# Kernel tuning notes

Hardware: AMD Instinct MI355X
Metric: run time of the kernel (lower is better)

## Reference

```python
import jax, jax.numpy as jnp
import numpy as np

E = 1024      # embedding_size
K = 64        # key_size
D = 64        # head_size
S = 1024      # context_size
V = 32000     # vocab_size
H = 16        # layer_size (heads per layer)
L = 8         # num_layers
B = 2


def _pe():
    pos = jnp.arange(S, dtype=jnp.float32)[:, None]
    i = jnp.arange(E, dtype=jnp.float32)[None, :]
    ang = pos / jnp.power(10000.0, 2.0 * i / E)
    return jnp.where((jnp.arange(E) % 2 == 0)[None, :], jnp.sin(ang), jnp.cos(ang))


def setup_inputs() -> dict:
    key = jax.random.key(0)
    ks = iter(jax.random.split(key, 32))
    s = 0.02
    n = lambda shape: jax.random.normal(next(ks), shape, dtype=jnp.float32) * s
    inp = {
        "tokens": jax.random.randint(next(ks), (B, S), 0, V),
        "emb": n((V, E)),
        "pe": _pe(),
        "k1w": n((L, H, K, E)), "k1b": n((L, H, K)),
        "k2w": n((L, H, K, K)), "k2b": n((L, H, K)),
        "q1w": n((L, H, K, E)), "q1b": n((L, H, K)),
        "q2w": n((L, H, K, K)), "q2b": n((L, H, K)),
        "vw": n((L, H, D, E)), "vb": n((L, H, D)),
        "lnw": jnp.ones((L, E), jnp.float32), "lnb": jnp.zeros((L, E), jnp.float32),
        "p1w": n((L, E, E)), "p1b": n((L, E)),
        "p2w": n((L, E, E)), "p2b": n((L, E)),
        "predw": n((V, E)), "predb": n((V,)),
    }
    return inp


def reference(tokens, emb, pe, k1w, k1b, k2w, k2b, q1w, q1b, q2w, q2b,
              vw, vb, lnw, lnb, p1w, p1b, p2w, p2b, predw, predb):
    relu = jax.nn.relu
    x = emb[tokens] + pe[:tokens.shape[1]]                       # [B,S,E]
    seq = tokens.shape[1]
    # Faithful to original: tril (past+diag) gets the -1e10 penalty.
    mask = jnp.tril(jnp.ones((seq, seq), x.dtype)) * -1e10
    for l in range(L):
        # two-layer ReLU MLPs for K and Q, batched over heads
        k = relu(jnp.einsum('bse,hke->bhsk', x, k1w[l]) + k1b[l][None, :, None, :])
        k = relu(jnp.einsum('bhsk,hjk->bhsj', k, k2w[l]) + k2b[l][None, :, None, :])
        q = relu(jnp.einsum('bse,hke->bhsk', x, q1w[l]) + q1b[l][None, :, None, :])
        q = relu(jnp.einsum('bhsk,hjk->bhsj', q, q2w[l]) + q2b[l][None, :, None, :])
        v = jnp.einsum('bse,hde->bhsd', x, vw[l]) + vb[l][None, :, None, :]
        scores = jnp.einsum('bhsk,bhtk->bhst', q, k) / (K ** 0.5) + mask
        w = jax.nn.softmax(scores, axis=-1)
        o = jnp.einsum('bhst,bhtd->bhsd', w, v)                  # [B,H,S,D]
        o = o.transpose(0, 2, 1, 3).reshape(x.shape[0], seq, H * D)
        y = x + o
        mu = y.mean(-1, keepdims=True)
        var = ((y - mu) ** 2).mean(-1, keepdims=True)
        yn = (y - mu) / jnp.sqrt(var + 1e-5) * lnw[l] + lnb[l]
        h1 = relu(yn @ p1w[l].T + p1b[l])
        x = relu(h1 @ p2w[l].T + p2b[l])
    logits = x @ predw.T + predb                                 # [B,S,V]
    return logits
```

## Files before the change

### kernel.cpp

```cpp
#include <hip/hip_runtime.h>


typedef __attribute__((ext_vector_type(8))) short bf16x8;
typedef __attribute__((ext_vector_type(4))) float f32x4;

#define L_ 8
#define S_ 1024
#define E_ 1024
#define B_ 2
#define H_ 16
#define V_ 32000
#define M_ 2048

__device__ __forceinline__ unsigned short f2b(float f) {
  union { float f; unsigned int u; } v; v.f = f;
  unsigned int r = v.u + 0x7FFFu + ((v.u >> 16) & 1u);
  return (unsigned short)(r >> 16);
}

#define GLDS16(gptr, lptr)                                                            \
  __builtin_amdgcn_global_load_lds(                                                   \
      (const __attribute__((address_space(1))) unsigned int*)(gptr),                  \
      (__attribute__((address_space(3))) unsigned int*)(lptr), 16, 0, 0)

__global__ void cvt_all_kernel(
    const float* __restrict__ k1w, const float* __restrict__ q1w,
    const float* __restrict__ vw,  const float* __restrict__ k2w,
    const float* __restrict__ q2w, const float* __restrict__ p1w,
    const float* __restrict__ p2w, const float* __restrict__ predw,
    unsigned short* __restrict__ wcat, unsigned short* __restrict__ wk2,
    unsigned short* __restrict__ wq2,  unsigned short* __restrict__ wp1,
    unsigned short* __restrict__ wp2,  unsigned short* __restrict__ wpred) {
  size_t u = (size_t)blockIdx.x * 256 + threadIdx.x;
  const float* src; unsigned short* dst;
  if (u < 6291456) {
    int seg = (int)(u / 2097152);
    size_t e0 = (u - (size_t)seg * 2097152) * 4;
    const float* s = (seg == 0) ? k1w : (seg == 1) ? q1w : vw;
    src = s + e0;
    int l = (int)(e0 >> 20), off = (int)(e0 & 1048575);
    dst = wcat + (size_t)l * 3145728 + (size_t)seg * 1048576 + off;
  } else if (u < 6422528) { size_t e = (u - 6291456) * 4;  src = k2w + e;   dst = wk2 + e; }
  else if (u < 6553600)   { size_t e = (u - 6422528) * 4;  src = q2w + e;   dst = wq2 + e; }
  else if (u < 8650752)   { size_t e = (u - 6553600) * 4;  src = p1w + e;   dst = wp1 + e; }
  else if (u < 10747904)  { size_t e = (u - 8650752) * 4;  src = p2w + e;   dst = wp2 + e; }
  else                    { size_t e = (u - 10747904) * 4; src = predw + e; dst = wpred + e; }
  float4 v = *(const float4*)src;
  dst[0] = f2b(v.x); dst[1] = f2b(v.y); dst[2] = f2b(v.z); dst[3] = f2b(v.w);
}

__global__ void biascat_kernel(const float* __restrict__ k1b, const float* __restrict__ q1b,
                               const float* __restrict__ vb, float* __restrict__ bcat) {
  int i = blockIdx.x * 256 + threadIdx.x;
  int l = i / 3072, j = i - l * 3072;
  float v;
  if (j < 1024)      v = k1b[l * 1024 + j];
  else if (j < 2048) v = q1b[l * 1024 + j - 1024];
  else               v = vb [l * 1024 + j - 2048];
  bcat[i] = v;
}

__global__ void embed_kernel(const int* __restrict__ tokens, const float* __restrict__ emb,
                             const float* __restrict__ pe, float* __restrict__ x32,
                             unsigned short* __restrict__ xb) {
  int row = blockIdx.x;
  int s = row & (S_ - 1);
  int e0 = threadIdx.x * 4;
  int tok = tokens[row];
  float4 ev = *(const float4*)(emb + (size_t)tok * E_ + e0);
  float4 pv = *(const float4*)(pe + (size_t)s * E_ + e0);
  float4 v; v.x = ev.x + pv.x; v.y = ev.y + pv.y; v.z = ev.z + pv.z; v.w = ev.w + pv.w;
  *(float4*)(x32 + (size_t)row * E_ + e0) = v;
  ushort4 o; o.x = f2b(v.x); o.y = f2b(v.y); o.z = f2b(v.z); o.w = f2b(v.w);
  *(ushort4*)(xb + (size_t)row * E_ + e0) = o;
}

template <int BM, int BN, int RELU, int OBF, int OF32, int VT>
__global__ __launch_bounds__(256) void gemm97(
    const unsigned short* __restrict__ A, const unsigned short* __restrict__ W,
    const float* __restrict__ bias, unsigned short* __restrict__ Cb,
    float* __restrict__ Cf, unsigned short* __restrict__ vTp,
    int K, int N, int reluN) {
  constexpr int AR = BM / 64;
  constexpr int BR = BN / 64;
  constexpr int FM = BM / 32;
  constexpr int FN = BN / 32;
  __shared__ __align__(16) unsigned short sA[BM * 32];
  __shared__ __align__(16) unsigned short sB[BN * 32];
  const int tid = threadIdx.x;
  const int lane = tid & 63, wave = tid >> 6;
  const int l16 = lane & 15, lhi = lane >> 4;

  const int gx = gridDim.x, nwg = gx * gridDim.y;
  int o = blockIdx.y * gx + blockIdx.x;
  int wg = ((nwg & 7) == 0) ? ((o & 7) * (nwg >> 3) + (o >> 3)) : o;
  const int row0 = (wg % gx) * BM, col0 = (wg / gx) * BN;

  const int wm = (wave >> 1) * (BM / 2), wn = (wave & 1) * (BN / 2);

  const int srow = wave * 16 + (lane >> 2);
  const int scol = ((lane & 3) ^ ((lane >> 3) & 3)) * 8;
  const int cx = (lhi ^ ((l16 >> 1) & 3)) * 8;

  f32x4 acc[FM][FN] = {};

  for (int k0 = 0; k0 < K; k0 += 32) {
#pragma unroll
    for (int r = 0; r < AR; r++)
      GLDS16(A + (size_t)(row0 + r * 64 + srow) * K + k0 + scol,
             sA + r * 2048 + wave * 512);
#pragma unroll
    for (int r = 0; r < BR; r++)
      GLDS16(W + (size_t)(col0 + r * 64 + srow) * K + k0 + scol,
             sB + r * 2048 + wave * 512);
    __syncthreads();

    bf16x8 af[FM], bf[FN];
#pragma unroll
    for (int i = 0; i < FM; i++)
      af[i] = *(const bf16x8*)(sA + (wm + i * 16 + l16) * 32 + cx);
#pragma unroll
    for (int j = 0; j < FN; j++)
      bf[j] = *(const bf16x8*)(sB + (wn + j * 16 + l16) * 32 + cx);
#pragma unroll
    for (int i = 0; i < FM; i++)
#pragma unroll
      for (int j = 0; j < FN; j++)
        acc[i][j] = __builtin_amdgcn_mfma_f32_16x16x32_bf16(bf[j], af[i], acc[i][j], 0, 0, 0);
    __syncthreads();
  }

#pragma unroll
  for (int j = 0; j < FN; j++) {
    const int colb = col0 + wn + j * 16 + lhi * 4;
    const float4 bv = *(const float4*)(bias + colb);
    const bool dorelu = (RELU == 1) || (RELU == 2 && colb < reluN);
#pragma unroll
    for (int i = 0; i < FM; i++) {
      const int row = row0 + wm + i * 16 + l16;
      float v0 = acc[i][j][0] + bv.x, v1 = acc[i][j][1] + bv.y;
      float v2 = acc[i][j][2] + bv.z, v3 = acc[i][j][3] + bv.w;
      if (dorelu) {
        v0 = fmaxf(v0, 0.f); v1 = fmaxf(v1, 0.f);
        v2 = fmaxf(v2, 0.f); v3 = fmaxf(v3, 0.f);
      }
      if (OBF) {
        ushort4 ob; ob.x = f2b(v0); ob.y = f2b(v1); ob.z = f2b(v2); ob.w = f2b(v3);
        *(ushort4*)(Cb + (size_t)row * N + colb) = ob;
      }
      if (OF32) {
        float4 of; of.x = v0; of.y = v1; of.z = v2; of.w = v3;
        *(float4*)(Cf + (size_t)row * N + colb) = of;
      }
      if (VT) {
        if (colb - lhi * 4 >= 2048) {
          const int hd0 = colb - 2048;
          const int bq = row >> 10, s = row & 1023;
          unsigned short* vr = vTp + ((size_t)(bq << 10) + hd0) * 1024 + s;
          vr[0] = f2b(v0); vr[1024] = f2b(v1); vr[2048] = f2b(v2); vr[3072] = f2b(v3);
        }
      }
    }
  }
}

__global__ __launch_bounds__(512, 1) void gemm256_8p(
    const unsigned short* __restrict__ A, const unsigned short* __restrict__ W,
    const float* __restrict__ bias, float* __restrict__ Cf) {
  constexpr int NT = 16;
  __shared__ __align__(16) unsigned short sA[2][2][8192];
  __shared__ __align__(16) unsigned short sB[2][2][8192];
  const int tid = threadIdx.x;
  const int lane = tid & 63, wave = tid >> 6;
  const int l16 = lane & 15, lhi = lane >> 4;
  const int wr = wave >> 2, wc = wave & 3;

  const int o = blockIdx.x;
  const int wg = (o & 7) * 125 + (o >> 3);
  const int row0 = (wg & 7) * 256;
  const int col0 = (wg >> 3) * 256;

  const int srow = tid >> 2;
  const int sk   = ((tid & 3) ^ ((tid >> 2) & 3)) * 8;
  const int rsw  = (l16 & 3);

  f32x4 acc[2][4][4] = {};

  auto stageA = [&](int kt, int s) {
    const int buf = kt & 1;
    const int kg = kt * 64 + s * 32 + sk;
#pragma unroll
    for (int i = 0; i < 2; i++)
      GLDS16(A + (size_t)(row0 + i * 128 + srow) * 1024 + kg,
             &sA[buf][s][i * 4096 + wave * 512]);
  };
  auto stageB = [&](int kt, int s) {
    const int buf = kt & 1;
    const int kg = kt * 64 + s * 32 + sk;
#pragma unroll
    for (int i = 0; i < 2; i++)
      GLDS16(W + (size_t)(col0 + i * 128 + srow) * 1024 + kg,
             &sB[buf][s][i * 4096 + wave * 512]);
  };

  stageA(0, 0); stageB(0, 0); stageA(0, 1); stageB(0, 1);

  bf16x8 af[4], bf[4];
  for (int kt = 0; kt < NT; kt++) {
    const int buf = kt & 1;
    const bool more = (kt + 1 < NT);

    asm volatile("s_waitcnt vmcnt(4)" ::: "memory");
    __builtin_amdgcn_s_barrier();
    __builtin_amdgcn_sched_barrier(0);
#pragma unroll
    for (int j = 0; j < 4; j++)
      bf[j] = *(const bf16x8*)(&sB[buf][0][(wc * 64 + j * 16 + l16) * 32 + ((lhi ^ rsw) << 3)]);
#pragma unroll
    for (int i = 0; i < 4; i++)
      af[i] = *(const bf16x8*)(&sA[buf][0][(wr * 128 + i * 16 + l16) * 32 + ((lhi ^ rsw) << 3)]);
    if (more) stageA(kt + 1, 0);
    asm volatile("s_waitcnt lgkmcnt(0)" ::: "memory");
    __builtin_amdgcn_sched_barrier(0);
    __builtin_amdgcn_s_setprio(1);
#pragma unroll
    for (int i = 0; i < 4; i++)
#pragma unroll
      for (int j = 0; j < 4; j++)
        acc[0][i][j] = __builtin_amdgcn_mfma_f32_16x16x32_bf16(bf[j], af[i], acc[0][i][j], 0, 0, 0);
    __builtin_amdgcn_s_setprio(0);
    __builtin_amdgcn_s_barrier();

#pragma unroll
    for (int i = 0; i < 4; i++)
      af[i] = *(const bf16x8*)(&sA[buf][0][(wr * 128 + 64 + i * 16 + l16) * 32 + ((lhi ^ rsw) << 3)]);
    if (more) stageB(kt + 1, 0);
    asm volatile("s_waitcnt lgkmcnt(0)" ::: "memory");
    __builtin_amdgcn_sched_barrier(0);
    __builtin_amdgcn_s_setprio(1);
#pragma unroll
    for (int i = 0; i < 4; i++)
#pragma unroll
      for (int j = 0; j < 4; j++)
        acc[1][i][j] = __builtin_amdgcn_mfma_f32_16x16x32_bf16(bf[j], af[i], acc[1][i][j], 0, 0, 0);
    __builtin_amdgcn_s_setprio(0);
    __builtin_amdgcn_s_barrier();

    if (kt == NT - 1) { asm volatile("s_waitcnt vmcnt(0)" ::: "memory"); }
    else              { asm volatile("s_waitcnt vmcnt(4)" ::: "memory"); }
    __builtin_amdgcn_s_barrier();
    __builtin_amdgcn_sched_barrier(0);
#pragma unroll
    for (int j = 0; j < 4; j++)
      bf[j] = *(const bf16x8*)(&sB[buf][1][(wc * 64 + j * 16 + l16) * 32 + ((lhi ^ rsw) << 3)]);
#pragma unroll
    for (int i = 0; i < 4; i++)
      af[i] = *(const bf16x8*)(&sA[buf][1][(wr * 128 + i * 16 + l16) * 32 + ((lhi ^ rsw) << 3)]);
    if (more) stageA(kt + 1, 1);
    asm volatile("s_waitcnt lgkmcnt(0)" ::: "memory");
    __builtin_amdgcn_sched_barrier(0);
    __builtin_amdgcn_s_setprio(1);
#pragma unroll
    for (int i = 0; i < 4; i++)
#pragma unroll
      for (int j = 0; j < 4; j++)
        acc[0][i][j] = __builtin_amdgcn_mfma_f32_16x16x32_bf16(bf[j], af[i], acc[0][i][j], 0, 0, 0);
    __builtin_amdgcn_s_setprio(0);
    __builtin_amdgcn_s_barrier();

#pragma unroll
    for (int i = 0; i < 4; i++)
      af[i] = *(const bf16x8*)(&sA[buf][1][(wr * 128 + 64 + i * 16 + l16) * 32 + ((lhi ^ rsw) << 3)]);
    if (more) stageB(kt + 1, 1);
    asm volatile("s_waitcnt lgkmcnt(0)" ::: "memory");
    __builtin_amdgcn_sched_barrier(0);
    __builtin_amdgcn_s_setprio(1);
#pragma unroll
    for (int i = 0; i < 4; i++)
#pragma unroll
      for (int j = 0; j < 4; j++)
        acc[1][i][j] = __builtin_amdgcn_mfma_f32_16x16x32_bf16(bf[j], af[i], acc[1][i][j], 0, 0, 0);
    __builtin_amdgcn_s_setprio(0);
    __builtin_amdgcn_s_barrier();
  }

#pragma unroll
  for (int rh = 0; rh < 2; rh++) {
#pragma unroll
    for (int j = 0; j < 4; j++) {
      const int colb = col0 + wc * 64 + j * 16 + lhi * 4;
      const float4 bv = *(const float4*)(bias + colb);
#pragma unroll
      for (int i = 0; i < 4; i++) {
        const int row = row0 + wr * 128 + rh * 64 + i * 16 + l16;
        float4 of;
        of.x = acc[rh][i][j][0] + bv.x; of.y = acc[rh][i][j][1] + bv.y;
        of.z = acc[rh][i][j][2] + bv.z; of.w = acc[rh][i][j][3] + bv.w;
        *(float4*)(Cf + (size_t)row * V_ + colb) = of;
      }
    }
  }
}

__global__ __launch_bounds__(256) void k2q2_kernel(
    const unsigned short* __restrict__ kqv, const unsigned short* __restrict__ wk2,
    const unsigned short* __restrict__ wq2, const float* __restrict__ k2b,
    const float* __restrict__ q2b, unsigned short* __restrict__ kbuf,
    unsigned short* __restrict__ qbuf) {
  const int m0 = blockIdx.x * 64;
  const int h = blockIdx.y;
  const int which = blockIdx.z;
  const unsigned short* Ap = kqv + (which ? 1024 : 0) + h * 64;
  const unsigned short* Wp = (which ? wq2 : wk2) + h * 4096;
  const float* bias = (which ? q2b : k2b) + h * 64;
  unsigned short* out = (which ? qbuf : kbuf) + h * 64;
  const int lane = threadIdx.x & 63, wave = threadIdx.x >> 6;
  const int l16 = lane & 15, lhi = lane >> 4;
  const int mw = m0 + wave * 16;

  f32x4 acc[4] = {};
#pragma unroll
  for (int ks = 0; ks < 2; ks++) {
    bf16x8 a = *(const bf16x8*)(Ap + (size_t)(mw + l16) * 3072 + ks * 32 + (lhi << 3));
#pragma unroll
    for (int j = 0; j < 4; j++) {
      bf16x8 b = *(const bf16x8*)(Wp + (j * 16 + l16) * 64 + ks * 32 + (lhi << 3));
      acc[j] = __builtin_amdgcn_mfma_f32_16x16x32_bf16(a, b, acc[j], 0, 0, 0);
    }
  }
#pragma unroll
  for (int j = 0; j < 4; j++) {
    float bv = bias[j * 16 + l16];
#pragma unroll
    for (int r = 0; r < 4; r++) {
      int row = mw + (lhi << 2) + r;
      float v = fmaxf(acc[j][r] + bv, 0.f);
      out[(size_t)row * 1024 + j * 16 + l16] = f2b(v);
    }
  }
}

__global__ __launch_bounds__(128) void attn_kernel(
    const unsigned short* __restrict__ qbuf,
    const unsigned short* __restrict__ kbuf,
    const unsigned short* __restrict__ vT,
    float* __restrict__ o32) {
  constexpr int LD = 72;
  __shared__ __align__(16) unsigned short sP[2 * 16 * LD];
  const int bid = blockIdx.x;
  const int bh = bid & 31, qt = bid >> 5;
  const int b = bh >> 4, h = bh & 15;
  const int tid = threadIdx.x, lane = tid & 63, w = tid >> 6;
  const int l16 = lane & 15, lhi = lane >> 4;
  const int base = b * S_;
  const int qrow = qt * 32 + w * 16 + l16;

  bf16x8 aq[2];
#pragma unroll
  for (int ks = 0; ks < 2; ks++)
    aq[ks] = *(const bf16x8*)(qbuf + (size_t)(base + qrow) * 1024 + h * 64 + ks * 32 + (lhi << 3));

  f32x4 oacc[4] = {};
  float psum[4] = {0.f, 0.f, 0.f, 0.f};
  const int srow = qt * 32 + w * 16 + (lhi << 2);
  const int t0s = (qt == 31) ? 0 : ((qt >> 1) << 6);

  unsigned short* sPw = sP + w * 16 * LD;

  bf16x8 kA[8], vA[8], kB[8], vB[8];

  auto loadKV = [&](int t0, bf16x8* kd, bf16x8* vd) {
#pragma unroll
    for (int nt = 0; nt < 4; nt++) {
#pragma unroll
      for (int ks = 0; ks < 2; ks++) {
        kd[nt * 2 + ks] = *(const bf16x8*)(kbuf + (size_t)(base + t0 + nt * 16 + l16) * 1024 +
                                           h * 64 + ks * 32 + (lhi << 3));
        vd[nt * 2 + ks] = *(const bf16x8*)(vT + (size_t)(bh * 64 + nt * 16 + l16) * 1024 +
                                           t0 + ks * 32 + (lhi << 3));
      }
    }
  };

  auto compute = [&](int t0, const bf16x8* kc, const bf16x8* vc) {
    f32x4 sacc[4] = {};
#pragma unroll
    for (int ks = 0; ks < 2; ks++)
#pragma unroll
      for (int nt = 0; nt < 4; nt++)
        sacc[nt] = __builtin_amdgcn_mfma_f32_16x16x32_bf16(aq[ks], kc[nt * 2 + ks], sacc[nt], 0, 0, 0);
#pragma unroll
    for (int nt = 0; nt < 4; nt++) {
      int tcol = t0 + nt * 16 + l16;
#pragma unroll
      for (int r = 0; r < 4; r++) {
        const int row = srow + r;
        float e;
        if (row == S_ - 1)      e = 1.f;
        else if (tcol <= row)   e = 0.f;
        else                    e = __expf(fminf(sacc[nt][r] * 0.125f, 60.f));
        psum[r] += e;
        sPw[((lhi << 2) + r) * LD + nt * 16 + l16] = f2b(e);
      }
    }
#pragma unroll
    for (int ks = 0; ks < 2; ks++) {
      bf16x8 ap = *(const bf16x8*)(sPw + l16 * LD + ks * 32 + (lhi << 3));
#pragma unroll
      for (int nt = 0; nt < 4; nt++)
        oacc[nt] = __builtin_amdgcn_mfma_f32_16x16x32_bf16(ap, vc[nt * 2 + ks], oacc[nt], 0, 0, 0);
    }
  };

  loadKV(t0s, kA, vA);
  int t0 = t0s;
  while (true) {
    if (t0 + 64 < S_) loadKV(t0 + 64, kB, vB);
    compute(t0, kA, vA);
    t0 += 64; if (t0 >= S_) break;
    if (t0 + 64 < S_) loadKV(t0 + 64, kA, vA);
    compute(t0, kB, vB);
    t0 += 64; if (t0 >= S_) break;
  }

  float lrun[4];
#pragma unroll
  for (int r = 0; r < 4; r++) {
    float rs = psum[r];
#pragma unroll
    for (int off = 1; off < 16; off <<= 1) rs += __shfl_xor(rs, off, 16);
    lrun[r] = rs;
  }
#pragma unroll
  for (int nt = 0; nt < 4; nt++) {
#pragma unroll
    for (int r = 0; r < 4; r++) {
      int row = srow + r;
      o32[(size_t)(base + row) * 1024 + h * 64 + nt * 16 + l16] = oacc[nt][r] / lrun[r];
    }
  }
}

__global__ __launch_bounds__(256) void ln_kernel(
    const float* __restrict__ x32, const float* __restrict__ o32,
    const float* __restrict__ lnw, const float* __restrict__ lnb,
    unsigned short* __restrict__ yn) {
  __shared__ float red[8];
  const int row = blockIdx.x, tid = threadIdx.x;
  const int lane = tid & 63, wave = tid >> 6;
  const int e0 = tid * 4;
  float4 xv = *(const float4*)(x32 + (size_t)row * E_ + e0);
  float4 ov = *(const float4*)(o32 + (size_t)row * E_ + e0);
  float y0 = xv.x + ov.x, y1 = xv.y + ov.y, y2 = xv.z + ov.z, y3 = xv.w + ov.w;
  float s = y0 + y1 + y2 + y3;
  float sq = y0 * y0 + y1 * y1 + y2 * y2 + y3 * y3;
#pragma unroll
  for (int off = 32; off > 0; off >>= 1) {
    s += __shfl_xor(s, off, 64);
    sq += __shfl_xor(sq, off, 64);
  }
  if (lane == 0) { red[wave * 2] = s; red[wave * 2 + 1] = sq; }
  __syncthreads();
  float ts = red[0] + red[2] + red[4] + red[6];
  float tsq = red[1] + red[3] + red[5] + red[7];
  float mu = ts * (1.f / E_);
  float var = tsq * (1.f / E_) - mu * mu;
  float rstd = rsqrtf(var + 1e-5f);
  float4 gv = *(const float4*)(lnw + e0);
  float4 bv = *(const float4*)(lnb + e0);
  ushort4 o;
  o.x = f2b((y0 - mu) * rstd * gv.x + bv.x);
  o.y = f2b((y1 - mu) * rstd * gv.y + bv.y);
  o.z = f2b((y2 - mu) * rstd * gv.z + bv.z);
  o.w = f2b((y3 - mu) * rstd * gv.w + bv.w);
  *(ushort4*)(yn + (size_t)row * E_ + e0) = o;
}

extern "C" void kernel_launch(void* const* d_in, const int* in_sizes, int n_in,
                              void* d_out, int out_size, void* d_ws, size_t ws_size,
                              hipStream_t stream) {
  const int* tokens  = (const int*)d_in[0];
  const float* emb   = (const float*)d_in[1];
  const float* pe    = (const float*)d_in[2];
  const float* k1w   = (const float*)d_in[3];
  const float* k1b   = (const float*)d_in[4];
  const float* k2w   = (const float*)d_in[5];
  const float* k2b   = (const float*)d_in[6];
  const float* q1w   = (const float*)d_in[7];
  const float* q1b   = (const float*)d_in[8];
  const float* q2w   = (const float*)d_in[9];
  const float* q2b   = (const float*)d_in[10];
  const float* vw    = (const float*)d_in[11];
  const float* vb    = (const float*)d_in[12];
  const float* lnw   = (const float*)d_in[13];
  const float* lnb   = (const float*)d_in[14];
  const float* p1w   = (const float*)d_in[15];
  const float* p1b   = (const float*)d_in[16];
  const float* p2w   = (const float*)d_in[17];
  const float* p2b   = (const float*)d_in[18];
  const float* predw = (const float*)d_in[19];
  const float* predb = (const float*)d_in[20];
  float* out = (float*)d_out;

  char* p = (char*)d_ws;
  auto alloc = [&](size_t bytes) -> char* {
    char* r = p; p += (bytes + 255) & ~(size_t)255; return r;
  };
  unsigned short* wcat  = (unsigned short*)alloc((size_t)L_ * 3072 * 1024 * 2);
  unsigned short* wk2   = (unsigned short*)alloc((size_t)L_ * H_ * 64 * 64 * 2);
  unsigned short* wq2   = (unsigned short*)alloc((size_t)L_ * H_ * 64 * 64 * 2);
  unsigned short* wp1   = (unsigned short*)alloc((size_t)L_ * 1024 * 1024 * 2);
  unsigned short* wp2   = (unsigned short*)alloc((size_t)L_ * 1024 * 1024 * 2);
  unsigned short* wpred = (unsigned short*)alloc((size_t)V_ * 1024 * 2);
  float*          bcat  = (float*)alloc((size_t)L_ * 3072 * 4);
  float*          x32   = (float*)alloc((size_t)M_ * 1024 * 4);
  unsigned short* xb    = (unsigned short*)alloc((size_t)M_ * 1024 * 2);
  unsigned short* kqv   = (unsigned short*)alloc((size_t)M_ * 3072 * 2);
  unsigned short* kbuf  = (unsigned short*)alloc((size_t)M_ * 1024 * 2);
  unsigned short* qbuf  = (unsigned short*)alloc((size_t)M_ * 1024 * 2);
  unsigned short* vTb   = (unsigned short*)alloc((size_t)32 * 64 * 1024 * 2);
  float*          o32   = (float*)alloc((size_t)M_ * 1024 * 4);
  unsigned short* yn    = (unsigned short*)alloc((size_t)M_ * 1024 * 2);
  unsigned short* h1    = (unsigned short*)alloc((size_t)M_ * 1024 * 2);
  if ((size_t)(p - (char*)d_ws) > ws_size) return;

  cvt_all_kernel<<<73984, 256, 0, stream>>>(k1w, q1w, vw, k2w, q2w, p1w, p2w, predw,
                                            wcat, wk2, wq2, wp1, wp2, wpred);
  biascat_kernel<<<96, 256, 0, stream>>>(k1b, q1b, vb, bcat);

  embed_kernel<<<M_, 256, 0, stream>>>(tokens, emb, pe, x32, xb);

  for (int l = 0; l < L_; l++) {
    const unsigned short* wcat_l = wcat + (size_t)l * 3072 * 1024;
    const float* bcat_l = bcat + (size_t)l * 3072;
    const unsigned short* wk2_l = wk2 + (size_t)l * H_ * 64 * 64;
    const unsigned short* wq2_l = wq2 + (size_t)l * H_ * 64 * 64;
    const unsigned short* wp1_l = wp1 + (size_t)l * 1024 * 1024;
    const unsigned short* wp2_l = wp2 + (size_t)l * 1024 * 1024;

    gemm97<128, 128, 2, 1, 0, 1><<<dim3(16, 24), 256, 0, stream>>>(
        xb, wcat_l, bcat_l, kqv, nullptr, vTb, 1024, 3072, 2048);
    k2q2_kernel<<<dim3(32, 16, 2), 256, 0, stream>>>(
        kqv, wk2_l, wq2_l, k2b + l * 1024, q2b + l * 1024, kbuf, qbuf);
    attn_kernel<<<1024, 128, 0, stream>>>(qbuf, kbuf, vTb, o32);
    ln_kernel<<<M_, 256, 0, stream>>>(x32, o32, lnw + l * 1024, lnb + l * 1024, yn);
    gemm97<64, 128, 1, 1, 0, 0><<<dim3(32, 8), 256, 0, stream>>>(
        yn, wp1_l, p1b + l * 1024, h1, nullptr, nullptr, 1024, 1024, 0);
    gemm97<64, 128, 1, 1, 1, 0><<<dim3(32, 8), 256, 0, stream>>>(
        h1, wp2_l, p2b + l * 1024, xb, x32, nullptr, 1024, 1024, 0);
  }

  gemm256_8p<<<1000, 512, 0, stream>>>(xb, wpred, predb, out);
}
```

Baseline: 1.457 ms.

## Fuse second K/Q MLP layer into the KQV projection GEMM epilogue

```diff
diff --git a/kernel.cpp b/kernel.cpp
--- a/kernel.cpp
+++ b/kernel.cpp
@@ -75,11 +75,14 @@
   *(ushort4*)(xb + (size_t)row * E_ + e0) = o;
 }
 
-template <int BM, int BN, int RELU, int OBF, int OF32, int VT>
+template <int BM, int BN, int RELU, int OBF, int OF32, int VT, int K2Q2>
 __global__ __launch_bounds__(256) void gemm97(
     const unsigned short* __restrict__ A, const unsigned short* __restrict__ W,
     const float* __restrict__ bias, unsigned short* __restrict__ Cb,
     float* __restrict__ Cf, unsigned short* __restrict__ vTp,
+    const unsigned short* __restrict__ wk2p, const unsigned short* __restrict__ wq2p,
+    const float* __restrict__ k2bp, const float* __restrict__ q2bp,
+    unsigned short* __restrict__ kbufp, unsigned short* __restrict__ qbufp,
     int K, int N, int reluN) {
   constexpr int AR = BM / 64;
   constexpr int BR = BN / 64;
@@ -87,6 +90,7 @@
   constexpr int FN = BN / 32;
   __shared__ __align__(16) unsigned short sA[BM * 32];
   __shared__ __align__(16) unsigned short sB[BN * 32];
+  __shared__ __align__(16) unsigned short sC[K2Q2 ? 128 * 136 : 1];
   const int tid = threadIdx.x;
   const int lane = tid & 63, wave = tid >> 6;
   const int l16 = lane & 15, lhi = lane >> 4;
@@ -130,34 +134,90 @@
     __syncthreads();
   }
 
-#pragma unroll
-  for (int j = 0; j < FN; j++) {
-    const int colb = col0 + wn + j * 16 + lhi * 4;
-    const float4 bv = *(const float4*)(bias + colb);
-    const bool dorelu = (RELU == 1) || (RELU == 2 && colb < reluN);
-#pragma unroll
-    for (int i = 0; i < FM; i++) {
-      const int row = row0 + wm + i * 16 + l16;
-      float v0 = acc[i][j][0] + bv.x, v1 = acc[i][j][1] + bv.y;
-      float v2 = acc[i][j][2] + bv.z, v3 = acc[i][j][3] + bv.w;
-      if (dorelu) {
-        v0 = fmaxf(v0, 0.f); v1 = fmaxf(v1, 0.f);
-        v2 = fmaxf(v2, 0.f); v3 = fmaxf(v3, 0.f);
+  if (K2Q2 && col0 < 2048) {
+#pragma unroll
+    for (int j = 0; j < FN; j++) {
+      const int colb = wn + j * 16 + lhi * 4;
+      const float4 bv = *(const float4*)(bias + col0 + colb);
+#pragma unroll
+      for (int i = 0; i < FM; i++) {
+        const int lrow = wm + i * 16 + l16;
+        ushort4 ob;
+        ob.x = f2b(fmaxf(acc[i][j][0] + bv.x, 0.f));
+        ob.y = f2b(fmaxf(acc[i][j][1] + bv.y, 0.f));
+        ob.z = f2b(fmaxf(acc[i][j][2] + bv.z, 0.f));
+        ob.w = f2b(fmaxf(acc[i][j][3] + bv.w, 0.f));
+        *(ushort4*)(sC + lrow * 136 + colb) = ob;
       }
-      if (OBF) {
-        ushort4 ob; ob.x = f2b(v0); ob.y = f2b(v1); ob.z = f2b(v2); ob.w = f2b(v3);
-        *(ushort4*)(Cb + (size_t)row * N + colb) = ob;
+    }
+    __syncthreads();
+    const int which = (col0 >= 1024) ? 1 : 0;
+    const int h = ((col0 & 1023) >> 6) + (wave & 1);
+    const unsigned short* W2 = (which ? wq2p : wk2p) + h * 4096;
+    const float* b2 = (which ? q2bp : k2bp) + h * 64;
+    unsigned short* outp = (which ? qbufp : kbufp) + h * 64;
+    const int r0 = (wave >> 1) * 64;
+    f32x4 acc2[4][4] = {};
+#pragma unroll
+    for (int ks = 0; ks < 2; ks++) {
+      bf16x8 bfr[4], af2[4];
+#pragma unroll
+      for (int j = 0; j < 4; j++)
+        bfr[j] = *(const bf16x8*)(W2 + (j * 16 + l16) * 64 + ks * 32 + (lhi << 3));
+#pragma unroll
+      for (int i = 0; i < 4; i++)
+        af2[i] = *(const bf16x8*)(sC + (r0 + i * 16 + l16) * 136 + (wave & 1) * 64 +
+                                  ks * 32 + (lhi << 3));
+#pragma unroll
+      for (int i = 0; i < 4; i++)
+#pragma unroll
+        for (int j = 0; j < 4; j++)
+          acc2[i][j] = __builtin_amdgcn_mfma_f32_16x16x32_bf16(bfr[j], af2[i], acc2[i][j], 0, 0, 0);
+    }
+#pragma unroll
+    for (int j = 0; j < 4; j++) {
+      const float4 bv = *(const float4*)(b2 + j * 16 + lhi * 4);
+#pragma unroll
+      for (int i = 0; i < 4; i++) {
+        const int row = row0 + r0 + i * 16 + l16;
+        ushort4 ob;
+        ob.x = f2b(fmaxf(acc2[i][j][0] + bv.x, 0.f));
+        ob.y = f2b(fmaxf(acc2[i][j][1] + bv.y, 0.f));
+        ob.z = f2b(fmaxf(acc2[i][j][2] + bv.z, 0.f));
+        ob.w = f2b(fmaxf(acc2[i][j][3] + bv.w, 0.f));
+        *(ushort4*)(outp + (size_t)row * 1024 + j * 16 + lhi * 4) = ob;
       }
-      if (OF32) {
-        float4 of; of.x = v0; of.y = v1; of.z = v2; of.w = v3;
-        *(float4*)(Cf + (size_t)row * N + colb) = of;
-      }
-      if (VT) {
-        if (colb - lhi * 4 >= 2048) {
-          const int hd0 = colb - 2048;
-          const int bq = row >> 10, s = row & 1023;
-          unsigned short* vr = vTp + ((size_t)(bq << 10) + hd0) * 1024 + s;
-          vr[0] = f2b(v0); vr[1024] = f2b(v1); vr[2048] = f2b(v2); vr[3072] = f2b(v3);
+    }
+  } else {
+#pragma unroll
+    for (int j = 0; j < FN; j++) {
+      const int colb = col0 + wn + j * 16 + lhi * 4;
+      const float4 bv = *(const float4*)(bias + colb);
+      const bool dorelu = (RELU == 1) || (RELU == 2 && colb < reluN);
+#pragma unroll
+      for (int i = 0; i < FM; i++) {
+        const int row = row0 + wm + i * 16 + l16;
+        float v0 = acc[i][j][0] + bv.x, v1 = acc[i][j][1] + bv.y;
+        float v2 = acc[i][j][2] + bv.z, v3 = acc[i][j][3] + bv.w;
+        if (dorelu) {
+          v0 = fmaxf(v0, 0.f); v1 = fmaxf(v1, 0.f);
+          v2 = fmaxf(v2, 0.f); v3 = fmaxf(v3, 0.f);
+        }
+        if (OBF) {
+          ushort4 ob; ob.x = f2b(v0); ob.y = f2b(v1); ob.z = f2b(v2); ob.w = f2b(v3);
+          *(ushort4*)(Cb + (size_t)row * N + colb) = ob;
+        }
+        if (OF32) {
+          float4 of; of.x = v0; of.y = v1; of.z = v2; of.w = v3;
+          *(float4*)(Cf + (size_t)row * N + colb) = of;
+        }
+        if (VT) {
+          if (colb - lhi * 4 >= 2048) {
+            const int hd0 = colb - 2048;
+            const int bq = row >> 10, s = row & 1023;
+            unsigned short* vr = vTp + ((size_t)(bq << 10) + hd0) * 1024 + s;
+            vr[0] = f2b(v0); vr[1024] = f2b(v1); vr[2048] = f2b(v2); vr[3072] = f2b(v3);
+          }
         }
       }
     }
@@ -181,8 +241,8 @@
   const int col0 = (wg >> 3) * 256;
 
   const int srow = tid >> 2;
-  const int sk   = ((tid & 3) ^ ((tid >> 2) & 3)) * 8;
-  const int rsw  = (l16 & 3);
+  const int sk   = ((tid & 3) ^ ((tid >> 3) & 3)) * 8;
+  const int rsw  = (l16 >> 1) & 3;
 
   f32x4 acc[2][4][4] = {};
 
@@ -298,44 +358,6 @@
         of.z = acc[rh][i][j][2] + bv.z; of.w = acc[rh][i][j][3] + bv.w;
         *(float4*)(Cf + (size_t)row * V_ + colb) = of;
       }
-    }
-  }
-}
-
-__global__ __launch_bounds__(256) void k2q2_kernel(
-    const unsigned short* __restrict__ kqv, const unsigned short* __restrict__ wk2,
-    const unsigned short* __restrict__ wq2, const float* __restrict__ k2b,
-    const float* __restrict__ q2b, unsigned short* __restrict__ kbuf,
-    unsigned short* __restrict__ qbuf) {
-  const int m0 = blockIdx.x * 64;
-  const int h = blockIdx.y;
-  const int which = blockIdx.z;
-  const unsigned short* Ap = kqv + (which ? 1024 : 0) + h * 64;
-  const unsigned short* Wp = (which ? wq2 : wk2) + h * 4096;
-  const float* bias = (which ? q2b : k2b) + h * 64;
-  unsigned short* out = (which ? qbuf : kbuf) + h * 64;
-  const int lane = threadIdx.x & 63, wave = threadIdx.x >> 6;
-  const int l16 = lane & 15, lhi = lane >> 4;
-  const int mw = m0 + wave * 16;
-
-  f32x4 acc[4] = {};
-#pragma unroll
-  for (int ks = 0; ks < 2; ks++) {
-    bf16x8 a = *(const bf16x8*)(Ap + (size_t)(mw + l16) * 3072 + ks * 32 + (lhi << 3));
-#pragma unroll
-    for (int j = 0; j < 4; j++) {
-      bf16x8 b = *(const bf16x8*)(Wp + (j * 16 + l16) * 64 + ks * 32 + (lhi << 3));
-      acc[j] = __builtin_amdgcn_mfma_f32_16x16x32_bf16(a, b, acc[j], 0, 0, 0);
-    }
-  }
-#pragma unroll
-  for (int j = 0; j < 4; j++) {
-    float bv = bias[j * 16 + l16];
-#pragma unroll
-    for (int r = 0; r < 4; r++) {
-      int row = mw + (lhi << 2) + r;
-      float v = fmaxf(acc[j][r] + bv, 0.f);
-      out[(size_t)row * 1024 + j * 16 + l16] = f2b(v);
     }
   }
 }
@@ -515,7 +537,6 @@
   float*          bcat  = (float*)alloc((size_t)L_ * 3072 * 4);
   float*          x32   = (float*)alloc((size_t)M_ * 1024 * 4);
   unsigned short* xb    = (unsigned short*)alloc((size_t)M_ * 1024 * 2);
-  unsigned short* kqv   = (unsigned short*)alloc((size_t)M_ * 3072 * 2);
   unsigned short* kbuf  = (unsigned short*)alloc((size_t)M_ * 1024 * 2);
   unsigned short* qbuf  = (unsigned short*)alloc((size_t)M_ * 1024 * 2);
   unsigned short* vTb   = (unsigned short*)alloc((size_t)32 * 64 * 1024 * 2);
@@ -538,16 +559,17 @@
     const unsigned short* wp1_l = wp1 + (size_t)l * 1024 * 1024;
     const unsigned short* wp2_l = wp2 + (size_t)l * 1024 * 1024;
 
-    gemm97<128, 128, 2, 1, 0, 1><<<dim3(16, 24), 256, 0, stream>>>(
-        xb, wcat_l, bcat_l, kqv, nullptr, vTb, 1024, 3072, 2048);
-    k2q2_kernel<<<dim3(32, 16, 2), 256, 0, stream>>>(
-        kqv, wk2_l, wq2_l, k2b + l * 1024, q2b + l * 1024, kbuf, qbuf);
+    gemm97<128, 128, 2, 0, 0, 1, 1><<<dim3(16, 24), 256, 0, stream>>>(
+        xb, wcat_l, bcat_l, nullptr, nullptr, vTb,
+        wk2_l, wq2_l, k2b + l * 1024, q2b + l * 1024, kbuf, qbuf, 1024, 3072, 2048);
     attn_kernel<<<1024, 128, 0, stream>>>(qbuf, kbuf, vTb, o32);
     ln_kernel<<<M_, 256, 0, stream>>>(x32, o32, lnw + l * 1024, lnb + l * 1024, yn);
-    gemm97<64, 128, 1, 1, 0, 0><<<dim3(32, 8), 256, 0, stream>>>(
-        yn, wp1_l, p1b + l * 1024, h1, nullptr, nullptr, 1024, 1024, 0);
-    gemm97<64, 128, 1, 1, 1, 0><<<dim3(32, 8), 256, 0, stream>>>(
-        h1, wp2_l, p2b + l * 1024, xb, x32, nullptr, 1024, 1024, 0);
+    gemm97<64, 128, 1, 1, 0, 0, 0><<<dim3(32, 8), 256, 0, stream>>>(
+        yn, wp1_l, p1b + l * 1024, h1, nullptr, nullptr,
+        nullptr, nullptr, nullptr, nullptr, nullptr, nullptr, 1024, 1024, 0);
+    gemm97<64, 128, 1, 1, 1, 0, 0><<<dim3(32, 8), 256, 0, stream>>>(
+        h1, wp2_l, p2b + l * 1024, xb, x32, nullptr,
+        nullptr, nullptr, nullptr, nullptr, nullptr, nullptr, 1024, 1024, 0);
   }
 
   gemm256_8p<<<1000, 512, 0, stream>>>(xb, wpred, predb, out);
```

New measurement: 1.396 ms. -4.2%, faster.
